# Kernel tuning notes

Measured on AMD Instinct MI355X. Metric: run time of the kernel, lower is better.

Reference implementation:

```python
import jax, jax.numpy as jnp
import numpy as np
from jax.ops import segment_sum

N_NODES = 50000
N_EDGES = 600000
IN_FEATS, N_HIDDEN, N_CLASSES = 128, 128, 16


def setup_inputs() -> dict:
    key = jax.random.key(0)
    ks = jax.random.split(key, 9)
    features = jax.random.normal(ks[0], (N_NODES, IN_FEATS), dtype=jnp.float32)
    src = jax.random.randint(ks[1], (N_EDGES,), 0, N_NODES, dtype=jnp.int32)
    dst = jax.random.randint(ks[2], (N_EDGES,), 0, N_NODES, dtype=jnp.int32)
    def glorot(k, fan_in, fan_out):
        s = jnp.sqrt(6.0 / (fan_in + fan_out))
        return jax.random.uniform(k, (fan_in, fan_out), jnp.float32, -s, s)
    W0 = glorot(ks[3], IN_FEATS, N_HIDDEN)
    b0 = jnp.zeros((N_HIDDEN,), jnp.float32)
    W1 = glorot(ks[4], N_HIDDEN, N_HIDDEN)
    b1 = jnp.zeros((N_HIDDEN,), jnp.float32)
    W2 = glorot(ks[5], N_HIDDEN, N_CLASSES)
    b2 = jnp.zeros((N_CLASSES,), jnp.float32)
    return {"features": features, "src": src, "dst": dst,
            "W0": W0, "b0": b0, "W1": W1, "b1": b1, "W2": W2, "b2": b2}


def _graph_conv(h, src, dst, norm_src, norm_dst, W, b, act):
    # DGL GraphConv, norm='both': act( D_in^{-1/2} A D_out^{-1/2} h W + b )
    h = h * norm_src  # [N, d_in]
    if W.shape[0] > W.shape[1]:
        # transform first when it shrinks the feature dim (DGL's optimization)
        h = h @ W
        agg = segment_sum(h[src], dst, num_segments=h.shape[0])  # SpMM
        out = agg * norm_dst + b
    else:
        agg = segment_sum(h[src], dst, num_segments=h.shape[0])  # SpMM
        out = (agg * norm_dst) @ W + b
    return act(out)


def reference(features, src, dst, W0, b0, W1, b1, W2, b2):
    n = features.shape[0]
    ones = jnp.ones((src.shape[0],), jnp.float32)
    deg_out = segment_sum(ones, src, num_segments=n)
    deg_in = segment_sum(ones, dst, num_segments=n)
    norm_src = jnp.where(deg_out > 0, jax.lax.rsqrt(jnp.maximum(deg_out, 1.0)), 0.0)[:, None]
    norm_dst = jnp.where(deg_in > 0, jax.lax.rsqrt(jnp.maximum(deg_in, 1.0)), 0.0)[:, None]
    relu = jax.nn.relu
    pos_sig = lambda x: jax.nn.sigmoid(x) + 1e-8
    h = _graph_conv(features, src, dst, norm_src, norm_dst, W0, b0, relu)
    h = _graph_conv(h, src, dst, norm_src, norm_dst, W1, b1, relu)
    h = _graph_conv(h, src, dst, norm_src, norm_dst, W2, b2, pos_sig)
    return h
```

## Files before the change

kernel.cpp:

```cpp
#include <hip/hip_runtime.h>
#include <hip/hip_bf16.h>


#define SCAN_TILE 1024

__global__ __launch_bounds__(256) void degree_kernel(
    const int* __restrict__ src, const int* __restrict__ dst,
    float* __restrict__ deg_out_f, int* __restrict__ cnt_in, int E) {
  int e = blockIdx.x * 256 + threadIdx.x;
  if (e < E) {
    atomicAdd(&deg_out_f[src[e]], 1.0f);
    atomicAdd(&cnt_in[dst[e]], 1);
  }
}

__global__ __launch_bounds__(256) void norm_kernel(
    float* __restrict__ ns, const int* __restrict__ cnt_in,
    float* __restrict__ nd, int n) {
  int i = blockIdx.x * 256 + threadIdx.x;
  if (i < n) {
    float v = ns[i];
    ns[i] = (v > 0.0f) ? rsqrtf(v) : 0.0f;
    int c = cnt_in[i];
    nd[i] = (c > 0) ? rsqrtf((float)c) : 0.0f;
  }
}

__global__ __launch_bounds__(256) void scan_blocksums(
    const int* __restrict__ cnt, int* __restrict__ bsum, int n) {
  const int t = threadIdx.x;
  const int base = blockIdx.x * SCAN_TILE + t * 4;
  int s = 0;
#pragma unroll
  for (int k = 0; k < 4; ++k) {
    int i = base + k;
    if (i < n) s += cnt[i];
  }
  __shared__ int red[256];
  red[t] = s;
  __syncthreads();
  for (int off = 128; off > 0; off >>= 1) {
    if (t < off) red[t] += red[t + off];
    __syncthreads();
  }
  if (t == 0) bsum[blockIdx.x] = red[0];
}

__global__ __launch_bounds__(256) void scan_bsums(
    int* __restrict__ bsum, int nb, int* __restrict__ rs_total) {
  __shared__ int sh[256];
  const int t = threadIdx.x;
  const int v = (t < nb) ? bsum[t] : 0;
  sh[t] = v;
  __syncthreads();
  for (int off = 1; off < 256; off <<= 1) {
    int u = (t >= off) ? sh[t - off] : 0;
    __syncthreads();
    sh[t] += u;
    __syncthreads();
  }
  if (t < nb) bsum[t] = sh[t] - v;
  if (t == 255) *rs_total = sh[255];
}

__global__ __launch_bounds__(256) void scan_final(
    const int* __restrict__ cnt, const int* __restrict__ bsum,
    int* __restrict__ row_start, int n) {
  const int t = threadIdx.x;
  const int base = blockIdx.x * SCAN_TILE + t * 4;
  int x[4];
#pragma unroll
  for (int k = 0; k < 4; ++k) {
    int i = base + k;
    x[k] = (i < n) ? cnt[i] : 0;
  }
  const int tsum = x[0] + x[1] + x[2] + x[3];
  __shared__ int sh[256];
  sh[t] = tsum;
  __syncthreads();
  for (int off = 1; off < 256; off <<= 1) {
    int u = (t >= off) ? sh[t - off] : 0;
    __syncthreads();
    sh[t] += u;
    __syncthreads();
  }
  int pre = sh[t] - tsum + bsum[blockIdx.x];
#pragma unroll
  for (int k = 0; k < 4; ++k) {
    int i = base + k;
    if (i < n) row_start[i] = pre;
    pre += x[k];
  }
}

__global__ __launch_bounds__(256) void scatter_kernel(
    const int* __restrict__ src, const int* __restrict__ dst,
    const int* __restrict__ row_start, int* __restrict__ cursor,
    int* __restrict__ col_idx, int E) {
  int e = blockIdx.x * 256 + threadIdx.x;
  if (e < E) {
    int d = dst[e];
    int pos = row_start[d] + atomicSub(&cursor[d], 1) - 1;
    col_idx[pos] = src[e];
  }
}

__global__ __launch_bounds__(256) void spmm128_csr(
    const float2* __restrict__ h2, const float* __restrict__ ns,
    const int* __restrict__ row_start, const int* __restrict__ col_idx,
    float2* __restrict__ agg2, int n) {
  const int node = blockIdx.x * 4 + (threadIdx.x >> 6);
  const int lane = threadIdx.x & 63;
  if (node >= n) return;
  const int beg = row_start[node];
  const int deg = row_start[node + 1] - beg;
  float2 acc = make_float2(0.f, 0.f);
  for (int base = 0; base < deg; base += 64) {
    const int m = min(64, deg - base);
    int colv = 0;
    float scv = 0.f;
    if (lane < m) {
      colv = col_idx[beg + base + lane];
      scv = ns[colv];
    }
    for (int j = 0; j < m; ++j) {
      int s = __shfl(colv, j);
      float sc = __shfl(scv, j);
      float2 v = h2[(size_t)s * 64 + lane];
      acc.x = fmaf(v.x, sc, acc.x);
      acc.y = fmaf(v.y, sc, acc.y);
    }
  }
  agg2[(size_t)node * 64 + lane] = acc;
}

__global__ __launch_bounds__(256) void spmm16_csr_fused(
    const float* __restrict__ t16,
    const int* __restrict__ row_start, const int* __restrict__ col_idx,
    const float* __restrict__ nd, const float* __restrict__ b2,
    float* __restrict__ out, int n) {
  const int idx = blockIdx.x * 256 + threadIdx.x;
  const int node = idx >> 4;
  const int lane = idx & 15;
  if (node >= n) return;
  const int beg = row_start[node];
  const int deg = row_start[node + 1] - beg;
  float acc = 0.f;
  for (int base = 0; base < deg; base += 16) {
    const int m = min(16, deg - base);
    int colv = 0;
    if (lane < m) colv = col_idx[beg + base + lane];
    for (int j = 0; j < m; ++j) {
      int s = __shfl(colv, j, 16);
      acc += t16[(size_t)s * 16 + lane];
    }
  }
  float v = acc * nd[node] + b2[lane];
  out[(size_t)node * 16 + lane] = 1.0f / (1.0f + expf(-v)) + 1e-8f;
}

__global__ __launch_bounds__(256) void gemm128_relu(
    const float* __restrict__ A, const float* __restrict__ nd,
    const float* __restrict__ Wg, const float* __restrict__ bias,
    float* __restrict__ C, int n) {
  __shared__ float4 Wt[32][32];
  __shared__ __align__(16) float At[32][32];
  const int row0 = blockIdx.x * 32;
  const int chunk = threadIdx.x & 31;
  const int rsub = threadIdx.x >> 5;
  const float4* A4 = (const float4*)A;
  const float4* W4 = (const float4*)Wg;

  const float4 bb = ((const float4*)bias)[chunk];
  float4 acc[4];
#pragma unroll
  for (int j = 0; j < 4; ++j) acc[j] = bb;

  for (int kt = 0; kt < 4; ++kt) {
    for (int i = threadIdx.x; i < 32 * 32; i += 256) {
      int k = i >> 5, c = i & 31;
      Wt[k][c] = W4[(size_t)(kt * 32 + k) * 32 + c];
    }
    {
      int i = threadIdx.x;
      int r = i >> 3, c4 = i & 7;
      int grow = row0 + r;
      float4 v = make_float4(0.f, 0.f, 0.f, 0.f);
      if (grow < n) {
        float s = nd[grow];
        v = A4[(size_t)grow * 32 + kt * 8 + c4];
        v.x *= s; v.y *= s; v.z *= s; v.w *= s;
      }
      ((float4*)At)[i] = v;
    }
    __syncthreads();
#pragma unroll
    for (int k = 0; k < 32; ++k) {
      float4 w = Wt[k][chunk];
#pragma unroll
      for (int j = 0; j < 4; ++j) {
        float a = At[rsub + 8 * j][k];
        acc[j].x = fmaf(a, w.x, acc[j].x);
        acc[j].y = fmaf(a, w.y, acc[j].y);
        acc[j].z = fmaf(a, w.z, acc[j].z);
        acc[j].w = fmaf(a, w.w, acc[j].w);
      }
    }
    __syncthreads();
  }
#pragma unroll
  for (int j = 0; j < 4; ++j) {
    int grow = row0 + rsub + 8 * j;
    if (grow < n) {
      float4 o = make_float4(fmaxf(acc[j].x, 0.f), fmaxf(acc[j].y, 0.f),
                             fmaxf(acc[j].z, 0.f), fmaxf(acc[j].w, 0.f));
      ((float4*)C)[(size_t)grow * 32 + chunk] = o;
    }
  }
}

__global__ __launch_bounds__(256) void transform16_kernel(
    const float* __restrict__ A, const float* __restrict__ ns,
    const float* __restrict__ W2, float* __restrict__ out, int n) {
  __shared__ float Wsh[128 * 16];
  __shared__ __align__(16) float Ash[16][128];
  const int row0 = blockIdx.x * 16;
  for (int i = threadIdx.x; i < 128 * 16; i += 256) Wsh[i] = W2[i];
  const float4* A4 = (const float4*)A;
  for (int i = threadIdx.x; i < 16 * 32; i += 256) {
    int r = i >> 5;
    int c = i & 31;
    int grow = row0 + r;
    float4 v = make_float4(0.f, 0.f, 0.f, 0.f);
    if (grow < n) {
      float s = ns[grow];
      v = A4[(size_t)grow * 32 + c];
      v.x *= s; v.y *= s; v.z *= s; v.w *= s;
    }
    ((float4*)Ash)[i] = v;
  }
  __syncthreads();
  int r = threadIdx.x >> 4, c = threadIdx.x & 15;
  float acc = 0.f;
#pragma unroll
  for (int k = 0; k < 128; ++k) acc = fmaf(Ash[r][k], Wsh[k * 16 + c], acc);
  int grow = row0 + r;
  if (grow < n) out[(size_t)grow * 16 + c] = acc;
}

extern "C" void kernel_launch(void* const* d_in, const int* in_sizes, int n_in,
                              void* d_out, int out_size, void* d_ws, size_t ws_size,
                              hipStream_t stream) {
  const float* features = (const float*)d_in[0];
  const int* src = (const int*)d_in[1];
  const int* dst = (const int*)d_in[2];
  const float* W0 = (const float*)d_in[3];
  const float* b0 = (const float*)d_in[4];
  const float* W1 = (const float*)d_in[5];
  const float* b1 = (const float*)d_in[6];
  const float* W2 = (const float*)d_in[7];
  const float* b2 = (const float*)d_in[8];
  float* out = (float*)d_out;

  const int n = in_sizes[0] / 128;
  const int E = in_sizes[1];

  float* ws = (float*)d_ws;
  float* bufA = ws;
  float* bufB = bufA + (size_t)n * 128;
  float* norm_src = bufB + (size_t)n * 128;
  int* cursor = (int*)(norm_src + n);
  float* norm_dst = (float*)(cursor + n);
  int* row_start = (int*)(norm_dst + n);
  int* col_idx = row_start + (n + 1);
  int* bsum = col_idx + E;

  const int nscan = (n + SCAN_TILE - 1) / SCAN_TILE;

  hipMemsetAsync(norm_src, 0, 2 * (size_t)n * sizeof(float), stream);
  degree_kernel<<<(E + 255) / 256, 256, 0, stream>>>(src, dst, norm_src, cursor, E);
  norm_kernel<<<(n + 255) / 256, 256, 0, stream>>>(norm_src, cursor, norm_dst, n);
  scan_blocksums<<<nscan, 256, 0, stream>>>(cursor, bsum, n);
  scan_bsums<<<1, 256, 0, stream>>>(bsum, nscan, row_start + n);
  scan_final<<<nscan, 256, 0, stream>>>(cursor, bsum, row_start, n);
  scatter_kernel<<<(E + 255) / 256, 256, 0, stream>>>(src, dst, row_start, cursor, col_idx, E);

  const int spmm_grid = (n + 3) / 4;
  const int gemm_grid = (n + 31) / 32;

  spmm128_csr<<<spmm_grid, 256, 0, stream>>>(
      (const float2*)features, norm_src, row_start, col_idx, (float2*)bufB, n);
  gemm128_relu<<<gemm_grid, 256, 0, stream>>>(bufB, norm_dst, W0, b0, bufA, n);

  spmm128_csr<<<spmm_grid, 256, 0, stream>>>(
      (const float2*)bufA, norm_src, row_start, col_idx, (float2*)bufB, n);
  gemm128_relu<<<gemm_grid, 256, 0, stream>>>(bufB, norm_dst, W1, b1, bufA, n);

  transform16_kernel<<<(n + 15) / 16, 256, 0, stream>>>(bufA, norm_src, W2, bufB, n);
  spmm16_csr_fused<<<(n * 16 + 255) / 256, 256, 0, stream>>>(
      bufB, row_start, col_idx, norm_dst, b2, out, n);
}
```

Baseline: 370.8 us.

## Replace global atomic degree counting with packed LDS histograms and reduction

Degree counting for src and dst moves from per-edge global atomics to per-block shared-memory histograms. Each 32-bit word packs two 16-bit counters, so a 50k-node histogram fits in LDS. 64 partial histograms per index array are written to scratch space borrowed from the feature buffers, and a reduce kernel sums them, computes both norms and writes the in-degree counts. This removes the memset, the global atomic contention and the separate norm kernel. The cost is the extra partial traffic, low occupancy from about 100KB of LDS per block, and a hard limit of NW_MAX nodes and of 65535 per-block counts in each 16-bit field.

```diff
diff --git a/kernel.cpp b/kernel.cpp
--- a/kernel.cpp
+++ b/kernel.cpp
@@ -3,27 +3,45 @@
 
 
 #define SCAN_TILE 1024
-
-__global__ __launch_bounds__(256) void degree_kernel(
-    const int* __restrict__ src, const int* __restrict__ dst,
-    float* __restrict__ deg_out_f, int* __restrict__ cnt_in, int E) {
-  int e = blockIdx.x * 256 + threadIdx.x;
-  if (e < E) {
-    atomicAdd(&deg_out_f[src[e]], 1.0f);
-    atomicAdd(&cnt_in[dst[e]], 1);
-  }
-}
-
-__global__ __launch_bounds__(256) void norm_kernel(
-    float* __restrict__ ns, const int* __restrict__ cnt_in,
-    float* __restrict__ nd, int n) {
-  int i = blockIdx.x * 256 + threadIdx.x;
-  if (i < n) {
-    float v = ns[i];
-    ns[i] = (v > 0.0f) ? rsqrtf(v) : 0.0f;
-    int c = cnt_in[i];
-    nd[i] = (c > 0) ? rsqrtf((float)c) : 0.0f;
-  }
+#define HIST_P    64
+#define NW_MAX    25088
+
+__global__ __launch_bounds__(256) void hist_pack(
+    const int* __restrict__ idx, unsigned* __restrict__ partials, int E, int nw) {
+  __shared__ unsigned sh[NW_MAX];
+  const int t = threadIdx.x;
+  for (int i = t; i < nw; i += 256) sh[i] = 0u;
+  __syncthreads();
+  const int per = (E + gridDim.x - 1) / gridDim.x;
+  const int beg = blockIdx.x * per;
+  const int end = min(E, beg + per);
+  for (int i = beg + t; i < end; i += 256) {
+    int v = idx[i];
+    atomicAdd(&sh[v >> 1], 1u << ((v & 1) * 16));
+  }
+  __syncthreads();
+  unsigned* outp = partials + (size_t)blockIdx.x * nw;
+  for (int i = t; i < nw; i += 256) outp[i] = sh[i];
+}
+
+__global__ __launch_bounds__(256) void reduce_hist(
+    const unsigned* __restrict__ pa, const unsigned* __restrict__ pb,
+    float* __restrict__ ns, float* __restrict__ nd, int* __restrict__ cnt, int nw) {
+  const int w = blockIdx.x * 256 + threadIdx.x;
+  if (w >= nw) return;
+  unsigned sa = 0, sb = 0;
+  for (int p = 0; p < HIST_P; ++p) {
+    sa += pa[(size_t)p * nw + w];
+    sb += pb[(size_t)p * nw + w];
+  }
+  unsigned a0 = sa & 0xffffu, a1 = sa >> 16;
+  unsigned b0 = sb & 0xffffu, b1 = sb >> 16;
+  ns[2 * w]     = a0 ? rsqrtf((float)a0) : 0.0f;
+  ns[2 * w + 1] = a1 ? rsqrtf((float)a1) : 0.0f;
+  nd[2 * w]     = b0 ? rsqrtf((float)b0) : 0.0f;
+  nd[2 * w + 1] = b1 ? rsqrtf((float)b1) : 0.0f;
+  cnt[2 * w] = (int)b0;
+  cnt[2 * w + 1] = (int)b1;
 }
 
 __global__ __launch_bounds__(256) void scan_blocksums(
@@ -95,12 +113,12 @@
 
 __global__ __launch_bounds__(256) void scatter_kernel(
     const int* __restrict__ src, const int* __restrict__ dst,
-    const int* __restrict__ row_start, int* __restrict__ cursor,
+    const int* __restrict__ row_start, int* __restrict__ cnt,
     int* __restrict__ col_idx, int E) {
   int e = blockIdx.x * 256 + threadIdx.x;
   if (e < E) {
     int d = dst[e];
-    int pos = row_start[d] + atomicSub(&cursor[d], 1) - 1;
+    int pos = row_start[d] + atomicSub(&cnt[d], 1) - 1;
     col_idx[pos] = src[e];
   }
 }
@@ -264,26 +282,30 @@
 
   const int n = in_sizes[0] / 128;
   const int E = in_sizes[1];
+  const int nw = (n + 1) / 2;
 
   float* ws = (float*)d_ws;
   float* bufA = ws;
   float* bufB = bufA + (size_t)n * 128;
   float* norm_src = bufB + (size_t)n * 128;
-  int* cursor = (int*)(norm_src + n);
-  float* norm_dst = (float*)(cursor + n);
+  int* cnt = (int*)(norm_src + n);
+  float* norm_dst = (float*)(cnt + n);
   int* row_start = (int*)(norm_dst + n);
   int* col_idx = row_start + (n + 1);
   int* bsum = col_idx + E;
+  unsigned* partialsA = (unsigned*)bufA;
+  unsigned* partialsB = (unsigned*)bufB;
 
   const int nscan = (n + SCAN_TILE - 1) / SCAN_TILE;
 
-  hipMemsetAsync(norm_src, 0, 2 * (size_t)n * sizeof(float), stream);
-  degree_kernel<<<(E + 255) / 256, 256, 0, stream>>>(src, dst, norm_src, cursor, E);
-  norm_kernel<<<(n + 255) / 256, 256, 0, stream>>>(norm_src, cursor, norm_dst, n);
-  scan_blocksums<<<nscan, 256, 0, stream>>>(cursor, bsum, n);
+  hist_pack<<<HIST_P, 256, 0, stream>>>(src, partialsA, E, nw);
+  hist_pack<<<HIST_P, 256, 0, stream>>>(dst, partialsB, E, nw);
+  reduce_hist<<<(nw + 255) / 256, 256, 0, stream>>>(
+      partialsA, partialsB, norm_src, norm_dst, cnt, nw);
+  scan_blocksums<<<nscan, 256, 0, stream>>>(cnt, bsum, n);
   scan_bsums<<<1, 256, 0, stream>>>(bsum, nscan, row_start + n);
-  scan_final<<<nscan, 256, 0, stream>>>(cursor, bsum, row_start, n);
-  scatter_kernel<<<(E + 255) / 256, 256, 0, stream>>>(src, dst, row_start, cursor, col_idx, E);
+  scan_final<<<nscan, 256, 0, stream>>>(cnt, bsum, row_start, n);
+  scatter_kernel<<<(E + 255) / 256, 256, 0, stream>>>(src, dst, row_start, cnt, col_idx, E);
 
   const int spmm_grid = (n + 3) / 4;
   const int gemm_grid = (n + 31) / 32;
```

Result: faster. 353.2 us (-4.7%).
